# Kernel tuning notes

Hardware: AMD Instinct MI355X
Metric: run time of the kernel (lower is better)

The kernel has to match this reference:

```python
import jax, jax.numpy as jnp
import numpy as np

B, C, H, W = 8, 256, 32, 32
N_HEADS, CH = 8, 32          # channel_head = channels // num_heads
HID = N_HEADS * CH           # hidden_channels


def setup_inputs() -> dict:
    key = jax.random.key(0)
    k1, k2, k3 = jax.random.split(key, 3)
    return {
        "x": jax.random.normal(k1, (B, C, H, W), dtype=jnp.float32),
        "w_qkv": jax.random.normal(k2, (3 * HID, C), dtype=jnp.float32) * 0.02,
        "b_qkv": jnp.zeros((3 * HID,), dtype=jnp.float32),
        "w_out": jax.random.normal(k3, (C, HID), dtype=jnp.float32) * 0.02,
        "b_out": jnp.zeros((C,), dtype=jnp.float32),
    }


def reference(x, w_qkv, b_qkv, w_out, b_out):
    b, c, h, w = x.shape
    s = h * w
    # qkv_conv: 1x1 conv + SiLU (norm='none' inside Conv2dBlock)
    qkv = jnp.einsum('bchw,oc->bohw', x, w_qkv) + b_qkv[None, :, None, None]
    qkv = jax.nn.silu(qkv)
    # rearrange 'b (n c) h w -> b n (3*ch) s' then chunk into q,k,v
    qkv = qkv.reshape(b, N_HEADS, 3 * CH, s)
    q, k, v = jnp.split(qkv, 3, axis=2)          # each [b, n, ch, s]
    # scores over flattened spatial positions, scaled by sqrt(channel_head)
    scores = jnp.einsum('bncs,bnct->bnst', q, k) / jnp.sqrt(jnp.float32(CH))
    attn = jax.nn.softmax(scores, axis=-1)        # softmax over key positions
    out = jnp.einsum('bnst,bnct->bncs', attn, v)  # [b, n, ch, s]
    out = out.reshape(b, N_HEADS * CH, h, w)      # 'b n c h w -> b (n c) h w'
    # out_conv: 1x1 conv, activation='none'
    out = jnp.einsum('bchw,oc->bohw', out, w_out) + b_out[None, :, None, None]
    # skip_connect=True, norm='none' => identity
    return out + x
```

## Files before the change

kernel.cpp:

```cpp
#include <hip/hip_runtime.h>
#include <math.h>

#define BB   8
#define NHD  8
#define SSZ  1024
#define CIN  256
#define HIDC 256

typedef __bf16 bf16_t;
typedef bf16_t bf16x8 __attribute__((ext_vector_type(8)));
typedef float  f32x4v __attribute__((ext_vector_type(4)));

typedef __attribute__((address_space(3))) unsigned short as3_u16;
typedef __attribute__((address_space(1))) unsigned short as1_u16;

__device__ inline unsigned cvt_pk_bf16(float lo, float hi) {
    unsigned r;
    asm("v_cvt_pk_bf16_f32 %0, %1, %2" : "=v"(r) : "v"(lo), "v"(hi));
    return r;
}
__device__ inline unsigned short f2bf(float f) {
    unsigned u = __builtin_bit_cast(unsigned, f);
    u = (u + 0x7fffu + ((u >> 16) & 1u)) >> 16;
    return (unsigned short)u;
}
__device__ inline float exp2_fast(float x) {
    float r;
    asm("v_exp_f32 %0, %1" : "=v"(r) : "v"(x));
    return r;
}
__device__ inline int kmap5(int i) {
    return ((i >> 2) & 3) * 8 + ((i >> 4) & 1) * 4 + (i & 3);
}

__global__ __launch_bounds__(256) void prepass(
    const float* __restrict__ x, const float* __restrict__ w_qkv,
    const float* __restrict__ w_out, unsigned short* __restrict__ Xt,
    unsigned short* __restrict__ Wq, unsigned short* __restrict__ Wo)
{
    const int tid = threadIdx.x;
    if (blockIdx.z == 8) {
        const int bid = blockIdx.y * 16 + blockIdx.x;
        const size_t base = (size_t)bid * 4096 + (size_t)tid * 16;
        #pragma unroll
        for (int i = 0; i < 4; ++i) {
            size_t idx = base + (size_t)i * 4;
            float4 v = (idx < 196608) ? *(const float4*)(w_qkv + idx)
                                      : *(const float4*)(w_out + (idx - 196608));
            ushort4 pk;
            pk.x = f2bf(v.x); pk.y = f2bf(v.y); pk.z = f2bf(v.z); pk.w = f2bf(v.w);
            if (idx < 196608) *(ushort4*)(Wq + idx) = pk;
            else              *(ushort4*)(Wo + (idx - 196608)) = pk;
        }
        return;
    }
    __shared__ unsigned short T[64][66];
    const int b = blockIdx.z, c0 = blockIdx.y * 64, s0 = blockIdx.x * 64;
    const float* xb = x + ((size_t)b * CIN + c0) * SSZ + s0;
    #pragma unroll
    for (int i = 0; i < 4; ++i) {
        int u = tid + i * 256;
        int c = u >> 4, s4 = u & 15;
        float4 v = *(const float4*)(xb + (size_t)c * SSZ + s4 * 4);
        T[s4 * 4 + 0][c] = f2bf(v.x);
        T[s4 * 4 + 1][c] = f2bf(v.y);
        T[s4 * 4 + 2][c] = f2bf(v.z);
        T[s4 * 4 + 3][c] = f2bf(v.w);
    }
    __syncthreads();
    unsigned short* dst = Xt + ((size_t)b << 18) + (size_t)s0 * 256 + c0;
    #pragma unroll
    for (int i = 0; i < 2; ++i) {
        int u = tid + i * 256;
        int s = u >> 3, c8 = u & 7;
        const unsigned* src = (const unsigned*)((const char*)&T[0][0] + s * 132 + c8 * 16);
        uint4 v = make_uint4(src[0], src[1], src[2], src[3]);
        *(uint4*)(dst + (size_t)s * 256 + c8 * 8) = v;
    }
}

#define QKV_LOAD(WF, XF, KK)                                                        \
    {                                                                               \
        _Pragma("unroll") for (int df = 0; df < 2; ++df)                            \
            WF[df] = *(const bf16x8*)(Wq + (size_t)(ob + df * 16 + ln) * 256 + (KK) + g * 8); \
        _Pragma("unroll") for (int sf = 0; sf < 4; ++sf)                            \
            XF[sf] = *(const bf16x8*)(Xb + (size_t)(sb + sf * 16 + ln) * 256 + (KK) + g * 8); \
    }
#define QKV_MMA(WF, XF)                                                             \
    {                                                                               \
        _Pragma("unroll") for (int df = 0; df < 2; ++df)                            \
            _Pragma("unroll") for (int sf = 0; sf < 4; ++sf)                        \
                acc[df][sf] = __builtin_amdgcn_mfma_f32_16x16x32_bf16(WF[df], XF[sf], acc[df][sf], 0, 0, 0); \
    }

__global__ __launch_bounds__(256) void qkv_mfma(
    const unsigned short* __restrict__ Wq, const unsigned short* __restrict__ Xt,
    const float* __restrict__ bias,
    unsigned short* __restrict__ qkT, unsigned short* __restrict__ v_buf)
{
    const int tid = threadIdx.x;
    const int l = tid & 63, w = tid >> 6;
    const int g = l >> 4, ln = l & 15;
    const int b  = blockIdx.z;
    const int ob = blockIdx.y * 64 + (w >> 1) * 32;
    const int sb = blockIdx.x * 128 + (w & 1) * 64;

    const unsigned short* Xb = Xt + ((size_t)b << 18);

    f32x4v acc[2][4];
    const f32x4v zero4 = {0.f, 0.f, 0.f, 0.f};
    #pragma unroll
    for (int df = 0; df < 2; ++df)
        #pragma unroll
        for (int sf = 0; sf < 4; ++sf) acc[df][sf] = zero4;

    bf16x8 wA[2], xA[4], wB[2], xB[4];
    QKV_LOAD(wA, xA, 0);
    #pragma unroll
    for (int k0 = 0; k0 < 256; k0 += 64) {
        if (k0 + 32 < 256) QKV_LOAD(wB, xB, k0 + 32);
        QKV_MMA(wA, xA);
        if (k0 + 64 < 256) QKV_LOAD(wA, xA, k0 + 64);
        QKV_MMA(wB, xB);
    }

    #pragma unroll
    for (int df = 0; df < 2; ++df) {
        const int o16  = ob + df * 16;
        const int part = (o16 >> 5) % 3;
        const int head = o16 / 96;
        const int bh   = b * NHD + head;
        const float4 b4 = *(const float4*)(bias + o16 + g * 4);
        const float bias_r[4] = {b4.x, b4.y, b4.z, b4.w};
        const int chb = (o16 & 31) + g * 4;

        float vals[4][4];
        #pragma unroll
        for (int sf = 0; sf < 4; ++sf)
            #pragma unroll
            for (int r = 0; r < 4; ++r) {
                float z = acc[df][sf][r] + bias_r[r];
                z = z / (1.f + __expf(-z));
                if (part == 0) z *= 0.25503482107810536f;
                vals[sf][r] = z;
            }

        if (part < 2) {
            const int slotb = ((chb >> 2) & 3) * 8 + ((chb >> 4) & 1) * 4;
            #pragma unroll
            for (int sf = 0; sf < 4; ++sf) {
                const int key = sb + sf * 16 + ln;
                ushort4 pk;
                pk.x = f2bf(vals[sf][0]); pk.y = f2bf(vals[sf][1]);
                pk.z = f2bf(vals[sf][2]); pk.w = f2bf(vals[sf][3]);
                *(ushort4*)(qkT + ((size_t)bh << 16) + (size_t)key * 64 + part * 32 + slotb) = pk;
            }
        } else {
            #pragma unroll
            for (int sf = 0; sf < 4; ++sf) {
                const int key  = sb + sf * 16 + ln;
                const int koff = (key & ~31) + kmap5(key & 31);
                #pragma unroll
                for (int r = 0; r < 4; ++r)
                    v_buf[((size_t)bh << 15) + ((size_t)(chb + r) << 10) + koff] = f2bf(vals[sf][r]);
            }
        }
    }
}

__global__ __launch_bounds__(256) void attn_mfma(
    const unsigned short* __restrict__ qkT,
    const unsigned short* __restrict__ v_buf,
    unsigned short* __restrict__ At)
{
    __shared__ unsigned short Ksh[4][2048];
    __shared__ unsigned short Vsh[4][2048];

    const int tid = threadIdx.x;
    const int l   = tid & 63;
    const int w   = tid >> 6;
    const int g   = l >> 4;
    const int ln  = l & 15;
    const int bh  = blockIdx.x;
    const int qt  = blockIdx.y;

    const unsigned short* qkrow = qkT   + ((size_t)bh << 16);
    const unsigned short* vb    = v_buf + ((size_t)bh << 15);

    const int q0 = qt * 64 + w * 16;

    const bf16x8 qf_ = *(const bf16x8*)(qkrow + (size_t)(q0 + ln) * 64 + g * 8);

    const bf16x8 ones = __builtin_bit_cast(bf16x8,
        make_uint4(0x3F803F80u, 0x3F803F80u, 0x3F803F80u, 0x3F803F80u));

    f32x4v O_[2], lacc;
    const f32x4v zero4 = {0.f, 0.f, 0.f, 0.f};
    O_[0] = zero4; O_[1] = zero4; lacc = zero4;

    const int krow = tid >> 2, ksl = tid & 3;
    const int vrow = tid >> 3, vsl = tid & 7;
    const unsigned short* gk_base = qkrow + (size_t)krow * 64 + 32 + ((ksl ^ ((krow >> 1) & 3)) << 3);
    const unsigned short* gv_base = vb + ((size_t)vrow << 10) + ((vsl ^ (vrow & 7)) << 3);
    const int wbase = w << 9;

#define STAGE_KV(BUF, T0)                                                          \
    {                                                                              \
        __builtin_amdgcn_global_load_lds((const as1_u16*)(gk_base + (size_t)(T0) * 64), \
                                         (as3_u16*)&Ksh[BUF][wbase], 16, 0, 0);    \
        __builtin_amdgcn_global_load_lds((const as1_u16*)(gv_base + (T0)),         \
                                         (as3_u16*)&Vsh[BUF][wbase], 16, 0, 0);    \
    }

    auto compute = [&](int cur) {
        const unsigned short* Kb = &Ksh[cur][0];
        const unsigned short* Vb = &Vsh[cur][0];
        bf16x8 kf_[4], vf_[2][2];
        #pragma unroll
        for (int kf = 0; kf < 4; ++kf)
            kf_[kf] = *(const bf16x8*)(Kb + ((kf * 16 + ln) << 5) + ((g ^ ((ln >> 1) & 3)) << 3));
        #pragma unroll
        for (int df = 0; df < 2; ++df)
            #pragma unroll
            for (int kb = 0; kb < 2; ++kb)
                vf_[df][kb] = *(const bf16x8*)(Vb + ((df * 16 + ln) << 6) + ((((kb << 2) + g) ^ (ln & 7)) << 3));

        f32x4v s_[4];
        __builtin_amdgcn_s_setprio(1);
        #pragma unroll
        for (int kf = 0; kf < 4; ++kf)
            s_[kf] = __builtin_amdgcn_mfma_f32_16x16x32_bf16(kf_[kf], qf_, zero4, 0, 0, 0);
        __builtin_amdgcn_s_setprio(0);

        #pragma unroll
        for (int kf = 0; kf < 4; ++kf)
            #pragma unroll
            for (int r = 0; r < 4; ++r)
                s_[kf][r] = exp2_fast(s_[kf][r]);

        __builtin_amdgcn_s_setprio(1);
        #pragma unroll
        for (int kb = 0; kb < 2; ++kb) {
            unsigned w0 = cvt_pk_bf16(s_[2 * kb][0],     s_[2 * kb][1]);
            unsigned w1 = cvt_pk_bf16(s_[2 * kb][2],     s_[2 * kb][3]);
            unsigned w2 = cvt_pk_bf16(s_[2 * kb + 1][0], s_[2 * kb + 1][1]);
            unsigned w3 = cvt_pk_bf16(s_[2 * kb + 1][2], s_[2 * kb + 1][3]);
            bf16x8 pf = __builtin_bit_cast(bf16x8, make_uint4(w0, w1, w2, w3));
            lacc = __builtin_amdgcn_mfma_f32_16x16x32_bf16(ones, pf, lacc, 0, 0, 0);
            #pragma unroll
            for (int df = 0; df < 2; ++df)
                O_[df] = __builtin_amdgcn_mfma_f32_16x16x32_bf16(vf_[df][kb], pf, O_[df], 0, 0, 0);
        }
        __builtin_amdgcn_s_setprio(0);
    };

    STAGE_KV(0, 0);
    STAGE_KV(1, 64);
    #pragma unroll
    for (int t = 0; t < 14; ++t) {
        STAGE_KV((t + 2) & 3, (t + 2) * 64);
        asm volatile("s_waitcnt vmcnt(4)" ::: "memory");
        __builtin_amdgcn_s_barrier();
        asm volatile("" ::: "memory");
        compute(t & 3);
        asm volatile("" ::: "memory");
    }
    asm volatile("s_waitcnt vmcnt(2)" ::: "memory");
    __builtin_amdgcn_s_barrier();
    asm volatile("" ::: "memory");
    compute(2);
    asm volatile("" ::: "memory");
    asm volatile("s_waitcnt vmcnt(0)" ::: "memory");
    __builtin_amdgcn_s_barrier();
    asm volatile("" ::: "memory");
    compute(3);

    const int b = bh >> 3, n = bh & 7;
    unsigned short* Ab = At + ((size_t)b << 18);
    const float inv = 1.f / lacc[0];
    const int qpos = q0 + ln;
    #pragma unroll
    for (int df = 0; df < 2; ++df) {
        ushort4 pk;
        pk.x = f2bf(O_[df][0] * inv);
        pk.y = f2bf(O_[df][1] * inv);
        pk.z = f2bf(O_[df][2] * inv);
        pk.w = f2bf(O_[df][3] * inv);
        *(ushort4*)(Ab + (size_t)qpos * 256 + n * 32 + df * 16 + g * 4) = pk;
    }
}

#define OUT_LOAD(WF, AF, KK)                                                        \
    {                                                                               \
        _Pragma("unroll") for (int df = 0; df < 2; ++df)                            \
            WF[df] = *(const bf16x8*)(Wo + (size_t)(ob + df * 16 + ln) * 256 + (KK) + g * 8); \
        _Pragma("unroll") for (int sf = 0; sf < 2; ++sf)                            \
            AF[sf] = *(const bf16x8*)(Ab + (size_t)(sb + sf * 16 + ln) * 256 + (KK) + g * 8); \
    }
#define OUT_MMA(WF, AF)                                                             \
    {                                                                               \
        _Pragma("unroll") for (int df = 0; df < 2; ++df)                            \
            _Pragma("unroll") for (int sf = 0; sf < 2; ++sf)                        \
                acc[df][sf] = __builtin_amdgcn_mfma_f32_16x16x32_bf16(WF[df], AF[sf], acc[df][sf], 0, 0, 0); \
    }

__global__ __launch_bounds__(256) void out_mfma(
    const unsigned short* __restrict__ Wo, const unsigned short* __restrict__ At,
    const float* __restrict__ bias, const float* __restrict__ x,
    float* __restrict__ out)
{
    const int tid = threadIdx.x;
    const int l = tid & 63, w = tid >> 6;
    const int g = l >> 4, ln = l & 15;
    const int b  = blockIdx.z;
    const int ob = blockIdx.y * 32;
    const int sb = blockIdx.x * 128 + w * 32;

    const unsigned short* Ab = At + ((size_t)b << 18);

    f32x4v acc[2][2];
    const f32x4v zero4 = {0.f, 0.f, 0.f, 0.f};
    #pragma unroll
    for (int df = 0; df < 2; ++df)
        #pragma unroll
        for (int sf = 0; sf < 2; ++sf) acc[df][sf] = zero4;

    bf16x8 wA[2], aA[2], wB[2], aB[2];
    OUT_LOAD(wA, aA, 0);
    #pragma unroll
    for (int k0 = 0; k0 < 256; k0 += 64) {
        if (k0 + 32 < 256) OUT_LOAD(wB, aB, k0 + 32);
        OUT_MMA(wA, aA);
        if (k0 + 64 < 256) OUT_LOAD(wA, aA, k0 + 64);
        OUT_MMA(wB, aB);
    }

    #pragma unroll
    for (int df = 0; df < 2; ++df) {
        const float4 b4 = *(const float4*)(bias + ob + df * 16 + g * 4);
        const float bias_r[4] = {b4.x, b4.y, b4.z, b4.w};
        #pragma unroll
        for (int sf = 0; sf < 2; ++sf) {
            const int s = sb + sf * 16 + ln;
            #pragma unroll
            for (int r = 0; r < 4; ++r) {
                const int o = ob + df * 16 + g * 4 + r;
                const size_t idx = ((size_t)b * CIN + o) * SSZ + s;
                out[idx] = acc[df][sf][r] + bias_r[r] + x[idx];
            }
        }
    }
}

extern "C" void kernel_launch(void* const* d_in, const int* in_sizes, int n_in,
                              void* d_out, int out_size, void* d_ws, size_t ws_size,
                              hipStream_t stream)
{
    const float* x     = (const float*)d_in[0];
    const float* w_qkv = (const float*)d_in[1];
    const float* b_qkv = (const float*)d_in[2];
    const float* w_out = (const float*)d_in[3];
    const float* b_out = (const float*)d_in[4];
    float* out = (float*)d_out;

    unsigned short* qkT   = (unsigned short*)d_ws;
    unsigned short* v_buf = qkT   + ((size_t)64 << 16);
    unsigned short* Xt    = v_buf + ((size_t)64 << 15);
    unsigned short* At    = Xt    + ((size_t)8 << 18);
    unsigned short* Wq    = At    + ((size_t)8 << 18);
    unsigned short* Wo    = Wq    + (size_t)768 * 256;

    prepass  <<<dim3(16, 4, 9),  256, 0, stream>>>(x, w_qkv, w_out, Xt, Wq, Wo);
    qkv_mfma <<<dim3(8, 12, 8),  256, 0, stream>>>(Wq, Xt, b_qkv, qkT, v_buf);
    attn_mfma<<<dim3(64, 16),    256, 0, stream>>>(qkT, v_buf, At);
    out_mfma <<<dim3(8, 8, 8),   256, 0, stream>>>(Wo, At, b_out, x, out);
}
```

Baseline: 57.19 us.

## Fuse fp32-to-bf16 prepass into QKV GEMM with swizzled LDS staging

Removes the separate prepass kernel. The QKV GEMM now reads fp32 x and w_qkv directly, converts them to bf16, and stages them in XOR-swizzled shared memory before the MFMA loop. The w_out conversion moves into an extra grid row of the same launch. This cuts one kernel launch and the global round trip through Xt/Wq. In exchange, each block re-converts its weight and x tiles redundantly and adds LDS staging with syncs, which may lower occupancy (64KB LDS per block).

```diff
diff --git a/kernel.cpp b/kernel.cpp
--- a/kernel.cpp
+++ b/kernel.cpp
@@ -33,58 +33,16 @@
     return ((i >> 2) & 3) * 8 + ((i >> 4) & 1) * 4 + (i & 3);
 }
 
-__global__ __launch_bounds__(256) void prepass(
-    const float* __restrict__ x, const float* __restrict__ w_qkv,
-    const float* __restrict__ w_out, unsigned short* __restrict__ Xt,
-    unsigned short* __restrict__ Wq, unsigned short* __restrict__ Wo)
-{
-    const int tid = threadIdx.x;
-    if (blockIdx.z == 8) {
-        const int bid = blockIdx.y * 16 + blockIdx.x;
-        const size_t base = (size_t)bid * 4096 + (size_t)tid * 16;
-        #pragma unroll
-        for (int i = 0; i < 4; ++i) {
-            size_t idx = base + (size_t)i * 4;
-            float4 v = (idx < 196608) ? *(const float4*)(w_qkv + idx)
-                                      : *(const float4*)(w_out + (idx - 196608));
-            ushort4 pk;
-            pk.x = f2bf(v.x); pk.y = f2bf(v.y); pk.z = f2bf(v.z); pk.w = f2bf(v.w);
-            if (idx < 196608) *(ushort4*)(Wq + idx) = pk;
-            else              *(ushort4*)(Wo + (idx - 196608)) = pk;
-        }
-        return;
-    }
-    __shared__ unsigned short T[64][66];
-    const int b = blockIdx.z, c0 = blockIdx.y * 64, s0 = blockIdx.x * 64;
-    const float* xb = x + ((size_t)b * CIN + c0) * SSZ + s0;
-    #pragma unroll
-    for (int i = 0; i < 4; ++i) {
-        int u = tid + i * 256;
-        int c = u >> 4, s4 = u & 15;
-        float4 v = *(const float4*)(xb + (size_t)c * SSZ + s4 * 4);
-        T[s4 * 4 + 0][c] = f2bf(v.x);
-        T[s4 * 4 + 1][c] = f2bf(v.y);
-        T[s4 * 4 + 2][c] = f2bf(v.z);
-        T[s4 * 4 + 3][c] = f2bf(v.w);
-    }
-    __syncthreads();
-    unsigned short* dst = Xt + ((size_t)b << 18) + (size_t)s0 * 256 + c0;
-    #pragma unroll
-    for (int i = 0; i < 2; ++i) {
-        int u = tid + i * 256;
-        int s = u >> 3, c8 = u & 7;
-        const unsigned* src = (const unsigned*)((const char*)&T[0][0] + s * 132 + c8 * 16);
-        uint4 v = make_uint4(src[0], src[1], src[2], src[3]);
-        *(uint4*)(dst + (size_t)s * 256 + c8 * 8) = v;
-    }
-}
-
-#define QKV_LOAD(WF, XF, KK)                                                        \
+#define QKV_LDS_LOAD(WF, XF, CB0)                                                   \
     {                                                                               \
-        _Pragma("unroll") for (int df = 0; df < 2; ++df)                            \
-            WF[df] = *(const bf16x8*)(Wq + (size_t)(ob + df * 16 + ln) * 256 + (KK) + g * 8); \
-        _Pragma("unroll") for (int sf = 0; sf < 4; ++sf)                            \
-            XF[sf] = *(const bf16x8*)(Xb + (size_t)(sb + sf * 16 + ln) * 256 + (KK) + g * 8); \
+        _Pragma("unroll") for (int df = 0; df < 2; ++df) {                          \
+            const int orow = (w >> 1) * 32 + df * 16 + ln;                          \
+            WF[df] = *(const bf16x8*)(Ws + orow * 256 + ((((CB0) + g) ^ (orow & 7)) << 3)); \
+        }                                                                           \
+        _Pragma("unroll") for (int sf = 0; sf < 4; ++sf) {                          \
+            const int srow = sbl + sf * 16 + ln;                                    \
+            XF[sf] = *(const bf16x8*)(Xs + srow * 128 + (((((CB0) & 15) + g) ^ (srow & 15)) << 3)); \
+        }                                                                           \
     }
 #define QKV_MMA(WF, XF)                                                             \
     {                                                                               \
@@ -93,19 +51,46 @@
                 acc[df][sf] = __builtin_amdgcn_mfma_f32_16x16x32_bf16(WF[df], XF[sf], acc[df][sf], 0, 0, 0); \
     }
 
-__global__ __launch_bounds__(256) void qkv_mfma(
-    const unsigned short* __restrict__ Wq, const unsigned short* __restrict__ Xt,
-    const float* __restrict__ bias,
-    unsigned short* __restrict__ qkT, unsigned short* __restrict__ v_buf)
+__global__ __launch_bounds__(256) void qkv_fused(
+    const float* __restrict__ W, const float* __restrict__ x,
+    const float* __restrict__ w_out, const float* __restrict__ bias,
+    unsigned short* __restrict__ qkT, unsigned short* __restrict__ v_buf,
+    unsigned short* __restrict__ Wo)
 {
+    __shared__ unsigned short Ws[64 * 256];
+    __shared__ unsigned short Xs[128 * 128];
+
     const int tid = threadIdx.x;
+
+    if (blockIdx.y == 12) {
+        const int chunk = blockIdx.z * 8 + blockIdx.x;
+        const size_t idx = (size_t)chunk * 1024 + (size_t)tid * 4;
+        float4 v = *(const float4*)(w_out + idx);
+        ushort4 pk;
+        pk.x = f2bf(v.x); pk.y = f2bf(v.y); pk.z = f2bf(v.z); pk.w = f2bf(v.w);
+        *(ushort4*)(Wo + idx) = pk;
+        return;
+    }
+
     const int l = tid & 63, w = tid >> 6;
     const int g = l >> 4, ln = l & 15;
     const int b  = blockIdx.z;
-    const int ob = blockIdx.y * 64 + (w >> 1) * 32;
-    const int sb = blockIdx.x * 128 + (w & 1) * 64;
-
-    const unsigned short* Xb = Xt + ((size_t)b << 18);
+    const int o0 = blockIdx.y * 64;
+    const int ob = o0 + (w >> 1) * 32;
+    const int s0 = blockIdx.x * 128;
+    const int sbl = (w & 1) * 64;
+
+    #pragma unroll
+    for (int it = 0; it < 16; ++it) {
+        const int u = it * 256 + tid;
+        const int row = u >> 6;
+        const int cq  = u & 63;
+        const float4 v = *(const float4*)(W + (size_t)(o0 + row) * 256 + cq * 4);
+        const int c  = cq * 4;
+        const int cbp = ((c >> 3) ^ (row & 7)) << 3;
+        unsigned two[2] = { cvt_pk_bf16(v.x, v.y), cvt_pk_bf16(v.z, v.w) };
+        *(uint2*)(Ws + row * 256 + cbp + (c & 7)) = *(uint2*)two;
+    }
 
     f32x4v acc[2][4];
     const f32x4v zero4 = {0.f, 0.f, 0.f, 0.f};
@@ -115,12 +100,36 @@
         for (int sf = 0; sf < 4; ++sf) acc[df][sf] = zero4;
 
     bf16x8 wA[2], xA[4], wB[2], xB[4];
-    QKV_LOAD(wA, xA, 0);
-    #pragma unroll
-    for (int k0 = 0; k0 < 256; k0 += 64) {
-        if (k0 + 32 < 256) QKV_LOAD(wB, xB, k0 + 32);
+
+    #pragma unroll
+    for (int h = 0; h < 2; ++h) {
+        if (h) __syncthreads();
+        #pragma unroll
+        for (int it = 0; it < 8; ++it) {
+            const int u  = it * 256 + tid;
+            const int cp = u >> 5;
+            const int sq = u & 31;
+            const float* r0 = x + ((size_t)b * CIN + h * 128 + 2 * cp) * SSZ + s0 + sq * 4;
+            const f32x4v a = *(const f32x4v*)r0;
+            const f32x4v d = *(const f32x4v*)(r0 + SSZ);
+            const int c_loc = 2 * cp;
+            const int cb    = c_loc >> 3;
+            #pragma unroll
+            for (int j = 0; j < 4; ++j) {
+                const int s_loc = sq * 4 + j;
+                const int elem  = s_loc * 128 + ((cb ^ (s_loc & 15)) << 3) + (c_loc & 7);
+                *(unsigned*)(Xs + elem) = cvt_pk_bf16(a[j], d[j]);
+            }
+        }
+        __syncthreads();
+
+        QKV_LDS_LOAD(wA, xA, h * 16 + 0);
+        QKV_LDS_LOAD(wB, xB, h * 16 + 4);
         QKV_MMA(wA, xA);
-        if (k0 + 64 < 256) QKV_LOAD(wA, xA, k0 + 64);
+        QKV_LDS_LOAD(wA, xA, h * 16 + 8);
+        QKV_MMA(wB, xB);
+        QKV_LDS_LOAD(wB, xB, h * 16 + 12);
+        QKV_MMA(wA, xA);
         QKV_MMA(wB, xB);
     }
 
@@ -149,7 +158,7 @@
             const int slotb = ((chb >> 2) & 3) * 8 + ((chb >> 4) & 1) * 4;
             #pragma unroll
             for (int sf = 0; sf < 4; ++sf) {
-                const int key = sb + sf * 16 + ln;
+                const int key = s0 + sbl + sf * 16 + ln;
                 ushort4 pk;
                 pk.x = f2bf(vals[sf][0]); pk.y = f2bf(vals[sf][1]);
                 pk.z = f2bf(vals[sf][2]); pk.w = f2bf(vals[sf][3]);
@@ -158,7 +167,7 @@
         } else {
             #pragma unroll
             for (int sf = 0; sf < 4; ++sf) {
-                const int key  = sb + sf * 16 + ln;
+                const int key  = s0 + sbl + sf * 16 + ln;
                 const int koff = (key & ~31) + kmap5(key & 31);
                 #pragma unroll
                 for (int r = 0; r < 4; ++r)
@@ -365,13 +374,10 @@
 
     unsigned short* qkT   = (unsigned short*)d_ws;
     unsigned short* v_buf = qkT   + ((size_t)64 << 16);
-    unsigned short* Xt    = v_buf + ((size_t)64 << 15);
-    unsigned short* At    = Xt    + ((size_t)8 << 18);
-    unsigned short* Wq    = At    + ((size_t)8 << 18);
-    unsigned short* Wo    = Wq    + (size_t)768 * 256;
-
-    prepass  <<<dim3(16, 4, 9),  256, 0, stream>>>(x, w_qkv, w_out, Xt, Wq, Wo);
-    qkv_mfma <<<dim3(8, 12, 8),  256, 0, stream>>>(Wq, Xt, b_qkv, qkT, v_buf);
-    attn_mfma<<<dim3(64, 16),    256, 0, stream>>>(qkT, v_buf, At);
-    out_mfma <<<dim3(8, 8, 8),   256, 0, stream>>>(Wo, At, b_out, x, out);
-}
+    unsigned short* At    = v_buf + ((size_t)64 << 15);
+    unsigned short* Wo    = At    + ((size_t)8 << 18);
+
+    qkv_fused<<<dim3(8, 13, 8), 256, 0, stream>>>(w_qkv, x, w_out, b_qkv, qkT, v_buf, Wo);
+    attn_mfma<<<dim3(64, 16),   256, 0, stream>>>(qkT, v_buf, At);
+    out_mfma <<<dim3(8, 8, 8),  256, 0, stream>>>(Wo, At, b_out, x, out);
+}
```

After: 52.54 us. 8.1% less time.
